# Performance work log

Measured on AMD Instinct MI355X. Metric: run time of the kernel, lower is better.

The kernel has to match this reference:

```python
import jax, jax.numpy as jnp
import numpy as np

B, S, D, H, L = 16, 1024, 512, 8, 3
NUM_Q, NUM_C, TOTAL_RES = 10000, 300, 2


def setup_inputs() -> dict:
    k = jax.random.split(jax.random.key(0), 20)
    n = lambda i, s, sc=0.02: jax.random.normal(k[i], s, jnp.float32) * sc
    z = lambda: jnp.zeros((D,), jnp.float32)
    o = lambda: jnp.ones((D,), jnp.float32)
    return {
        'in_ex': jax.random.randint(k[0], (B, S), 0, NUM_Q),
        'in_cat': jax.random.randint(k[1], (B, S), 0, NUM_C),
        'in_res': jax.random.randint(k[2], (B, S), 0, 2),
        'in_pos': n(3, (B, S, D)),
        'en_out': n(4, (B, S, D)),
        'E_res': n(5, (TOTAL_RES + 1, D)),
        'E_ex': n(6, (2 * NUM_Q + 1, D)),
        'E_cat': n(7, (2 * NUM_C + 1, D)),
        'g1': o(), 'be1': z(), 'g2': o(), 'be2': z(), 'g3': o(), 'be3': z(),
        'Wq1': n(8, (D, D)), 'bq1': z(), 'Wk1': n(9, (D, D)), 'bk1': z(),
        'Wv1': n(10, (D, D)), 'bv1': z(), 'Wo1': n(11, (D, D)), 'bo1': z(),
        'Wq2': n(12, (D, D)), 'bq2': z(), 'Wk2': n(13, (D, D)), 'bk2': z(),
        'Wv2': n(14, (D, D)), 'bv2': z(), 'Wo2': n(15, (D, D)), 'bo2': z(),
        'fW1': n(16, (D, D)), 'fb1': z(), 'fW2': n(17, (D, D)), 'fb2': z(),
    }


def layer_norm(x, g, b, eps=1e-5):
    m = x.mean(-1, keepdims=True)
    v = ((x - m) ** 2).mean(-1, keepdims=True)
    return (x - m) / jnp.sqrt(v + eps) * g + b


def pyr_attn(q_in, kv_in, Wq, bq, Wk, bk, Wv, bv, Wo, bo):
    # q_in, kv_in: (S, B, D) as in nn.MultiheadAttention convention
    Sq, Bq, Dm = q_in.shape
    dh = Dm // H
    heads = lambda x: x.reshape(x.shape[0], Bq, H, dh).transpose(1, 2, 0, 3)  # (B,H,S,dh)
    qh = heads(q_in @ Wq + bq)
    kh = heads(kv_in @ Wk + bk)
    vh = heads(kv_in @ Wv + bv)
    Skv = kv_in.shape[0]
    i = jnp.arange(Sq)[:, None]
    Ks, Vs, Ms = [], [], []
    for l in range(L):  # pyramid levels: keys/values avg-pooled by 2**l
        f = 2 ** l
        nb = Skv // f
        Ks.append(kh[:, :, :nb * f].reshape(Bq, H, nb, f, dh).mean(3))
        Vs.append(vh[:, :, :nb * f].reshape(Bq, H, nb, f, dh).mean(3))
        # causal: query i may attend pooled block j only if the block ends at or before i
        Ms.append(i >= (jnp.arange(nb)[None, :] + 1) * f - 1)
    K = jnp.concatenate(Ks, 2)
    V = jnp.concatenate(Vs, 2)
    M = jnp.concatenate(Ms, 1)  # (Sq, K_total) multi-level causal mask
    sc = jnp.einsum('bhqd,bhkd->bhqk', qh, K) / np.sqrt(dh).astype(np.float32)
    sc = jnp.where(M[None, None], sc, -1e9)
    a = jax.nn.softmax(sc, -1)
    out = jnp.einsum('bhqk,bhkd->bhqd', a, V)
    return out.transpose(2, 0, 1, 3).reshape(Sq, Bq, Dm) @ Wo + bo


def reference(in_ex, in_cat, in_res, in_pos, en_out, E_res, E_ex, E_cat,
              g1, be1, g2, be2, g3, be3,
              Wq1, bq1, Wk1, bk1, Wv1, bv1, Wo1, bo1,
              Wq2, bq2, Wk2, bk2, Wv2, bv2, Wo2, bo2,
              fW1, fb1, fW2, fb2):
    # embedding sum (first_block=True)
    out = E_res[in_res] + E_ex[in_ex + NUM_Q * in_res] + E_cat[in_cat + NUM_C * in_res] + in_pos
    out = out.transpose(1, 0, 2)  # (S, B, D)
    out = layer_norm(out, g1, be1)
    out = out + pyr_attn(out, out, Wq1, bq1, Wk1, bk1, Wv1, bv1, Wo1, bo1)
    en = layer_norm(en_out.transpose(1, 0, 2), g2, be2)
    out = out + pyr_attn(out, en, Wq2, bq2, Wk2, bk2, Wv2, bv2, Wo2, bo2)
    out = out.transpose(1, 0, 2)  # (B, S, D)
    out = layer_norm(out, g3, be3)
    out = out + (jax.nn.relu(out @ fW1 + fb1) @ fW2 + fb2)
    return out
```

## Files before the change

kernel.cpp:

```cpp
#include <hip/hip_runtime.h>


#define BB 16
#define SS 1024
#define DD 512
#define HH 8
#define DH 64
#define KTOT 1792
#define NROW (BB*SS)

typedef unsigned short u16;
typedef __attribute__((ext_vector_type(8))) u16 u16x8;
typedef __attribute__((ext_vector_type(4))) u16 u16x4;
typedef __attribute__((ext_vector_type(8))) short s16x8;
typedef __attribute__((ext_vector_type(4))) float f32x4;

__device__ __forceinline__ float b2f(u16 u) {
    return __uint_as_float(((unsigned int)u) << 16);
}
__device__ __forceinline__ u16 f2b(float f) {
    unsigned int u = __float_as_uint(f);
    return (u16)((u + 0x7FFF + ((u >> 16) & 1)) >> 16);
}
__device__ __forceinline__ s16x8 u2s8(u16x8 u) {
    union { u16x8 u; s16x8 s; } x; x.u = u; return x.s;
}
__device__ __forceinline__ f32x4 mfma16(s16x8 a, s16x8 b, f32x4 c) {
    return __builtin_amdgcn_mfma_f32_16x16x32_bf16(a, b, c, 0, 0, 0);
}
__device__ __forceinline__ float wave_sum(float v) {
    #pragma unroll
    for (int m = 1; m < 64; m <<= 1) v += __shfl_xor(v, m, 64);
    return v;
}

__global__ __launch_bounds__(256) void embed_ln_k(
    const int* __restrict__ in_ex, const int* __restrict__ in_cat,
    const int* __restrict__ in_res, const float* __restrict__ in_pos,
    const float* __restrict__ E_res, const float* __restrict__ E_ex,
    const float* __restrict__ E_cat, const float* __restrict__ g,
    const float* __restrict__ be, float* __restrict__ out)
{
    int wave = threadIdx.x >> 6, lane = threadIdx.x & 63;
    int row = blockIdx.x * 4 + wave;
    int res = in_res[row];
    int ex  = in_ex[row] + 10000 * res;
    int cat = in_cat[row] + 300 * res;
    int d0 = lane * 8;
    const float* pr = &E_res[(size_t)res * DD + d0];
    const float* pe = &E_ex[(size_t)ex * DD + d0];
    const float* pc = &E_cat[(size_t)cat * DD + d0];
    const float* pp = &in_pos[(size_t)row * DD + d0];
    float x[8]; float s = 0.f;
    #pragma unroll
    for (int j = 0; j < 8; j++) { x[j] = pr[j] + pe[j] + pc[j] + pp[j]; s += x[j]; }
    s = wave_sum(s);
    float mean = s * (1.0f / DD);
    float vs = 0.f;
    #pragma unroll
    for (int j = 0; j < 8; j++) { float d = x[j] - mean; vs += d * d; }
    vs = wave_sum(vs);
    float rstd = rsqrtf(vs * (1.0f / DD) + 1e-5f);
    #pragma unroll
    for (int j = 0; j < 8; j++)
        out[(size_t)row * DD + d0 + j] = (x[j] - mean) * rstd * g[d0 + j] + be[d0 + j];
}

template<bool OUTB>
__global__ __launch_bounds__(256) void ln_k(
    const float* __restrict__ x, const float* __restrict__ g,
    const float* __restrict__ be, void* __restrict__ outv)
{
    int wave = threadIdx.x >> 6, lane = threadIdx.x & 63;
    int row = blockIdx.x * 4 + wave;
    int d0 = lane * 8;
    const float* px = &x[(size_t)row * DD + d0];
    float xv[8]; float s = 0.f;
    #pragma unroll
    for (int j = 0; j < 8; j++) { xv[j] = px[j]; s += xv[j]; }
    s = wave_sum(s);
    float mean = s * (1.0f / DD);
    float vs = 0.f;
    #pragma unroll
    for (int j = 0; j < 8; j++) { float d = xv[j] - mean; vs += d * d; }
    vs = wave_sum(vs);
    float rstd = rsqrtf(vs * (1.0f / DD) + 1e-5f);
    #pragma unroll
    for (int j = 0; j < 8; j++) {
        float v = (xv[j] - mean) * rstd * g[d0 + j] + be[d0 + j];
        if (OUTB) ((u16*)outv)[(size_t)row * DD + d0 + j] = f2b(v);
        else      ((float*)outv)[(size_t)row * DD + d0 + j] = v;
    }
}

__global__ __launch_bounds__(256) void transpose_k(const float* __restrict__ src, u16* __restrict__ dst)
{
    int idx = blockIdx.x * 256 + threadIdx.x;
    int n = idx & 511, k = idx >> 9;
    dst[n * 512 + k] = f2b(src[k * 512 + n]);
}

__global__ __launch_bounds__(256) void pool_k12_k(u16* __restrict__ KP)
{
    int idx = blockIdx.x * 256 + threadIdx.x;
    int d = idx & 63;
    int t = idx >> 6;
    int k12 = t % 768;
    int bh = t / 768;
    int s0, f;
    if (k12 < 512) { s0 = 2 * k12; f = 2; } else { s0 = 4 * (k12 - 512); f = 4; }
    size_t base = (size_t)bh * KTOT * DH;
    float acc = 0.f;
    for (int i = 0; i < f; i++)
        acc += b2f(KP[base + (size_t)(s0 + i) * DH + d]);
    KP[base + (size_t)(1024 + k12) * DH + d] = f2b(acc * (1.0f / (float)f));
}

__global__ __launch_bounds__(256) void pool_vt_k(const u16* __restrict__ Vp, u16* __restrict__ VPt)
{
    __shared__ __align__(16) u16 T[64 * 72];
    int tid = threadIdx.x;
    int st = blockIdx.x;
    int h  = blockIdx.y;
    int b  = blockIdx.z;
    int s0 = st * 64;
    {
        const u16* src = &Vp[((size_t)(b * SS + s0)) * DD + h * DH];
        #pragma unroll
        for (int it = 0; it < 2; it++) {
            int idx = it * 256 + tid;
            int row = idx >> 3, unit = idx & 7;
            *(u16x8*)&T[row * 72 + unit * 8] =
                *(const u16x8*)&src[(size_t)row * DD + unit * 8];
        }
    }
    __syncthreads();
    int d = tid & 63, g = tid >> 6;
    size_t obase = ((size_t)(b * HH + h) * DH + d) * KTOT;
    #pragma unroll
    for (int gg = 0; gg < 2; gg++) {
        int grp = g * 2 + gg;
        u16x8 v;
        #pragma unroll
        for (int j = 0; j < 8; j++) v[j] = T[(grp * 8 + j) * 72 + d];
        *(u16x8*)&VPt[obase + s0 + grp * 8] = v;
    }
    {
        u16x8 v;
        #pragma unroll
        for (int j = 0; j < 8; j++) {
            int sl = g * 8 + j;
            float a = b2f(T[(2 * sl) * 72 + d]) + b2f(T[(2 * sl + 1) * 72 + d]);
            v[j] = f2b(a * 0.5f);
        }
        *(u16x8*)&VPt[obase + 1024 + st * 32 + g * 8] = v;
    }
    {
        u16x4 v;
        #pragma unroll
        for (int j = 0; j < 4; j++) {
            int s2 = g * 4 + j;
            float a = 0.f;
            #pragma unroll
            for (int i = 0; i < 4; i++) a += b2f(T[(4 * s2 + i) * 72 + d]);
            v[j] = f2b(a * 0.25f);
        }
        *(u16x4*)&VPt[obase + 1536 + st * 16 + g * 4] = v;
    }
}

template<bool AF32, bool RELU, bool RES, bool OUTB, bool KLAY>
__global__ __launch_bounds__(256) void gemm_k(
    const void* __restrict__ Av, const u16* __restrict__ Wt,
    const float* __restrict__ bias, const float* __restrict__ resid,
    void* __restrict__ Cv, int M, int K)
{
    const int N = 512;
    __shared__ __align__(16) u16 As[128 * 40];
    __shared__ __align__(16) u16 Bs[128 * 40];
    int tid = threadIdx.x;
    int wave = tid >> 6, lane = tid & 63;
    int quad = lane >> 4, l16 = lane & 15;
    int m0 = blockIdx.y * 128, n0 = blockIdx.x * 128;
    int wm = (wave >> 1) * 64, wn = (wave & 1) * 64;
    int r = tid >> 1, cg = (tid & 1) * 16;
    f32x4 acc[4][4];
    #pragma unroll
    for (int i = 0; i < 4; i++)
        #pragma unroll
        for (int j = 0; j < 4; j++)
            #pragma unroll
            for (int rr = 0; rr < 4; rr++) acc[i][j][rr] = 0.f;

    for (int k0 = 0; k0 < K; k0 += 32) {
        __syncthreads();
        if (AF32) {
            const float* src = &((const float*)Av)[(size_t)(m0 + r) * K + k0 + cg];
            u16x8 lo, hi;
            #pragma unroll
            for (int j = 0; j < 8; j++) { lo[j] = f2b(src[j]); hi[j] = f2b(src[j + 8]); }
            *(u16x8*)&As[r * 40 + cg] = lo;
            *(u16x8*)&As[r * 40 + cg + 8] = hi;
        } else {
            const u16* src = &((const u16*)Av)[(size_t)(m0 + r) * K + k0 + cg];
            *(u16x8*)&As[r * 40 + cg] = *(const u16x8*)&src[0];
            *(u16x8*)&As[r * 40 + cg + 8] = *(const u16x8*)&src[8];
        }
        {
            const u16* src = &Wt[(size_t)(n0 + r) * K + k0 + cg];
            *(u16x8*)&Bs[r * 40 + cg] = *(const u16x8*)&src[0];
            *(u16x8*)&Bs[r * 40 + cg + 8] = *(const u16x8*)&src[8];
        }
        __syncthreads();
        s16x8 af[4], bfr[4];
        #pragma unroll
        for (int i = 0; i < 4; i++)
            af[i] = u2s8(*(const u16x8*)&As[(wm + i * 16 + l16) * 40 + quad * 8]);
        #pragma unroll
        for (int j = 0; j < 4; j++)
            bfr[j] = u2s8(*(const u16x8*)&Bs[(wn + j * 16 + l16) * 40 + quad * 8]);
        #pragma unroll
        for (int i = 0; i < 4; i++)
            #pragma unroll
            for (int j = 0; j < 4; j++)
                acc[i][j] = mfma16(af[i], bfr[j], acc[i][j]);
    }

    #pragma unroll
    for (int j = 0; j < 4; j++) {
        int col = n0 + wn + j * 16 + l16;
        float bv = bias[col];
        #pragma unroll
        for (int i = 0; i < 4; i++) {
            int rowb = m0 + wm + i * 16 + quad * 4;
            #pragma unroll
            for (int rr = 0; rr < 4; rr++) {
                float v = acc[i][j][rr] + bv;
                if (RELU) v = fmaxf(v, 0.f);
                int row = rowb + rr;
                if (RES) v += resid[(size_t)row * N + col];
                if (KLAY) {
                    int b_ = row >> 10, s_ = row & 1023;
                    size_t dst = (((size_t)(b_ * HH + (col >> 6)) * KTOT) + s_) * DH + (col & 63);
                    ((u16*)Cv)[dst] = f2b(v);
                } else if (OUTB) {
                    ((u16*)Cv)[(size_t)row * N + col] = f2b(v);
                } else {
                    ((float*)Cv)[(size_t)row * N + col] = v;
                }
            }
        }
    }
}

__global__ __launch_bounds__(512) void attn_k(
    const u16* __restrict__ Qp, const u16* __restrict__ KP,
    const u16* __restrict__ VPt, u16* __restrict__ Hout)
{
    __shared__ __align__(16) u16 Ksh[64 * 72];
    __shared__ __align__(16) u16 Vsh[64 * 72];
    __shared__ float Sc[8][16 * 68];
    int tid = threadIdx.x;
    int wave = tid >> 6, lane = tid & 63;
    int quad = lane >> 4, l16 = lane & 15;
    int id = blockIdx.x;
    int h = id & 7;
    int inner = id >> 3;
    int x = inner & 3, b = inner >> 2;

    int t0 = x + 4 * wave;
    int tiles[2] = { t0, 63 - t0 };

    const u16* Kb = KP  + ((size_t)(b * HH + h)) * KTOT * DH;
    const u16* Vt = VPt + ((size_t)(b * HH + h)) * DH * KTOT;

    s16x8 qa[2][2];
    f32x4 o[2][4];
    float mrun[2] = {-INFINITY, -INFINITY}, lrun[2] = {0.f, 0.f};
    #pragma unroll
    for (int c = 0; c < 2; c++) {
        int q0 = tiles[c] * 16;
        const u16* qrow = Qp + ((size_t)(b * SS + q0 + l16)) * DD + h * DH;
        qa[c][0] = u2s8(*(const u16x8*)&qrow[quad * 8]);
        qa[c][1] = u2s8(*(const u16x8*)&qrow[32 + quad * 8]);
        #pragma unroll
        for (int j = 0; j < 4; j++)
            #pragma unroll
            for (int r = 0; r < 4; r++) o[c][j][r] = 0.f;
    }
    float* Sw = &Sc[wave][0];

    int srow = tid >> 3, sunit = tid & 7;
    u16x8 kreg = *(const u16x8*)&Kb[(size_t)tid * 8];
    u16x8 vreg = *(const u16x8*)&Vt[(size_t)srow * KTOT + sunit * 8];

    for (int ch = 0; ch < 28; ch++) {
        int kbase = ch * 64;
        int lv = (ch < 16) ? 0 : (ch < 24) ? 1 : 2;
        __syncthreads();
        *(u16x8*)&Ksh[srow * 72 + sunit * 8] = kreg;
        *(u16x8*)&Vsh[srow * 72 + sunit * 8] = vreg;
        __syncthreads();
        if (ch + 1 < 28) {
            int nb = (ch + 1) * 64;
            kreg = *(const u16x8*)&Kb[(size_t)nb * DH + tid * 8];
            vreg = *(const u16x8*)&Vt[(size_t)srow * KTOT + nb + sunit * 8];
        }

        #pragma unroll
        for (int c = 0; c < 2; c++) {
            int q0 = tiles[c] * 16;
            int qmax = q0 + 15;
            int efirst = (lv == 0) ? kbase
                       : (lv == 1) ? 2 * (kbase - 1024) + 1
                                   : 4 * (kbase - 1536) + 3;
            if (efirst > qmax) continue;

            #pragma unroll
            for (int t = 0; t < 4; t++) {
                const u16* kr = &Ksh[(t * 16 + l16) * 72];
                s16x8 kf0 = u2s8(*(const u16x8*)&kr[quad * 8]);
                s16x8 kf1 = u2s8(*(const u16x8*)&kr[32 + quad * 8]);
                f32x4 z;
                #pragma unroll
                for (int r = 0; r < 4; r++) z[r] = 0.f;
                z = mfma16(qa[c][0], kf0, z);
                z = mfma16(qa[c][1], kf1, z);
                int key = kbase + t * 16 + l16;
                int e = (lv == 0) ? key
                      : (lv == 1) ? 2 * (key - 1024) + 1
                                  : 4 * (key - 1536) + 3;
                #pragma unroll
                for (int r = 0; r < 4; r++) {
                    int q = q0 + quad * 4 + r;
                    Sw[(quad * 4 + r) * 68 + t * 16 + l16] =
                        (q >= e) ? z[r] * 0.125f : -1e30f;
                }
            }
            asm volatile("s_waitcnt lgkmcnt(0)" ::: "memory");

            float sv[16];
            {
                const float* base0 = &Sw[l16 * 68 + quad * 8];
                f32x4 a0 = *(const f32x4*)&base0[0];
                f32x4 a1 = *(const f32x4*)&base0[4];
                f32x4 a2 = *(const f32x4*)&base0[32];
                f32x4 a3 = *(const f32x4*)&base0[36];
                #pragma unroll
                for (int j = 0; j < 4; j++) {
                    sv[j] = a0[j]; sv[4 + j] = a1[j];
                    sv[8 + j] = a2[j]; sv[12 + j] = a3[j];
                }
            }

            float cmax = sv[0];
            #pragma unroll
            for (int j = 1; j < 16; j++) cmax = fmaxf(cmax, sv[j]);
            cmax = fmaxf(cmax, __shfl_xor(cmax, 16, 64));
            cmax = fmaxf(cmax, __shfl_xor(cmax, 32, 64));
            float newm = fmaxf(mrun[c], cmax);
            float al = __expf(mrun[c] - newm);
            float p[16]; float ps = 0.f;
            #pragma unroll
            for (int j = 0; j < 16; j++) { p[j] = __expf(sv[j] - newm); ps += p[j]; }
            ps += __shfl_xor(ps, 16, 64);
            ps += __shfl_xor(ps, 32, 64);
            lrun[c] = lrun[c] * al + ps;
            mrun[c] = newm;

            float alr[4];
            #pragma unroll
            for (int r = 0; r < 4; r++) alr[r] = __shfl(al, quad * 4 + r, 64);
            #pragma unroll
            for (int j = 0; j < 4; j++)
                #pragma unroll
                for (int r = 0; r < 4; r++) o[c][j][r] *= alr[r];

            u16x8 pk0, pk1;
            #pragma unroll
            for (int j = 0; j < 8; j++) { pk0[j] = f2b(p[j]); pk1[j] = f2b(p[8 + j]); }
            s16x8 pf0 = u2s8(pk0), pf1 = u2s8(pk1);

            #pragma unroll
            for (int j = 0; j < 4; j++) {
                const u16* vr = &Vsh[(j * 16 + l16) * 72];
                o[c][j] = mfma16(pf0, u2s8(*(const u16x8*)&vr[quad * 8]), o[c][j]);
                o[c][j] = mfma16(pf1, u2s8(*(const u16x8*)&vr[32 + quad * 8]), o[c][j]);
            }
        }
    }

    #pragma unroll
    for (int c = 0; c < 2; c++) {
        int q0 = tiles[c] * 16;
        float il = 1.0f / lrun[c];
        float ilr[4];
        #pragma unroll
        for (int r = 0; r < 4; r++) ilr[r] = __shfl(il, quad * 4 + r, 64);
        #pragma unroll
        for (int r = 0; r < 4; r++) {
            int q = q0 + quad * 4 + r;
            #pragma unroll
            for (int j = 0; j < 4; j++)
                Hout[((size_t)(b * SS + q)) * DD + h * DH + j * 16 + l16] = f2b(o[c][j][r] * ilr[r]);
        }
    }
}

extern "C" void kernel_launch(void* const* d_in, const int* in_sizes, int n_in,
                              void* d_out, int out_size, void* d_ws, size_t ws_size,
                              hipStream_t stream)
{
    (void)in_sizes; (void)n_in; (void)out_size; (void)ws_size;
    const int* in_ex  = (const int*)d_in[0];
    const int* in_cat = (const int*)d_in[1];
    const int* in_res = (const int*)d_in[2];
    const float* in_pos = (const float*)d_in[3];
    const float* en_out = (const float*)d_in[4];
    const float* E_res  = (const float*)d_in[5];
    const float* E_ex   = (const float*)d_in[6];
    const float* E_cat  = (const float*)d_in[7];
    const float* g1 = (const float*)d_in[8],  *be1 = (const float*)d_in[9];
    const float* g2 = (const float*)d_in[10], *be2 = (const float*)d_in[11];
    const float* g3 = (const float*)d_in[12], *be3 = (const float*)d_in[13];
    const float* Wq1 = (const float*)d_in[14], *bq1 = (const float*)d_in[15];
    const float* Wk1 = (const float*)d_in[16], *bk1 = (const float*)d_in[17];
    const float* Wv1 = (const float*)d_in[18], *bv1 = (const float*)d_in[19];
    const float* Wo1 = (const float*)d_in[20], *bo1 = (const float*)d_in[21];
    const float* Wq2 = (const float*)d_in[22], *bq2 = (const float*)d_in[23];
    const float* Wk2 = (const float*)d_in[24], *bk2 = (const float*)d_in[25];
    const float* Wv2 = (const float*)d_in[26], *bv2 = (const float*)d_in[27];
    const float* Wo2 = (const float*)d_in[28], *bo2 = (const float*)d_in[29];
    const float* fW1 = (const float*)d_in[30], *fb1 = (const float*)d_in[31];
    const float* fW2 = (const float*)d_in[32], *fb2 = (const float*)d_in[33];

    char* ws = (char*)d_ws;
    const size_t U = (size_t)NROW * DD * 2;
    float* x1 = (float*)(ws);
    u16* qb   = (u16*)(ws + 2 * U);
    u16* vb   = (u16*)(ws + 3 * U);
    u16* hb   = (u16*)(ws + 4 * U);
    u16* kp   = (u16*)(ws + 5 * U);
    u16* vpt  = (u16*)(ws + 5 * U + 7 * U / 4);
    u16* wt   = (u16*)(ws + 8 * U + U / 2);
    float* x2 = (float*)d_out;
    u16* en = (u16*)(ws);
    float* x3 = x1;
    float* x4 = (float*)(ws + 5 * U);
    u16* ff1 = hb;

    const float* wsrc[10] = {Wq1, Wk1, Wv1, Wo1, Wq2, Wk2, Wv2, Wo2, fW1, fW2};
    for (int i = 0; i < 10; i++)
        transpose_k<<<1024, 256, 0, stream>>>(wsrc[i], wt + (size_t)i * 262144);
    u16* tWq1 = wt,            *tWk1 = wt + 262144,   *tWv1 = wt + 2*262144, *tWo1 = wt + 3*262144;
    u16* tWq2 = wt + 4*262144, *tWk2 = wt + 5*262144, *tWv2 = wt + 6*262144, *tWo2 = wt + 7*262144;
    u16* tF1  = wt + 8*262144, *tF2  = wt + 9*262144;

    dim3 ggrid(4, 128);
    dim3 vtgrid(16, 8, 16);

    embed_ln_k<<<4096, 256, 0, stream>>>(in_ex, in_cat, in_res, in_pos,
                                         E_res, E_ex, E_cat, g1, be1, x1);

    gemm_k<true,false,false,true,false><<<ggrid, 256, 0, stream>>>(x1, tWq1, bq1, nullptr, qb, NROW, 512);
    gemm_k<true,false,false,true,true ><<<ggrid, 256, 0, stream>>>(x1, tWk1, bk1, nullptr, kp, NROW, 512);
    gemm_k<true,false,false,true,false><<<ggrid, 256, 0, stream>>>(x1, tWv1, bv1, nullptr, vb, NROW, 512);
    pool_k12_k<<<24576, 256, 0, stream>>>(kp);
    pool_vt_k<<<vtgrid, 256, 0, stream>>>(vb, vpt);
    attn_k<<<512, 512, 0, stream>>>(qb, kp, vpt, hb);
    gemm_k<false,false,true,false,false><<<ggrid, 256, 0, stream>>>(hb, tWo1, bo1, x1, x2, NROW, 512);

    ln_k<true><<<4096, 256, 0, stream>>>(en_out, g2, be2, en);
    gemm_k<true,false,false,true,false><<<ggrid, 256, 0, stream>>>(x2, tWq2, bq2, nullptr, qb, NROW, 512);
    gemm_k<false,false,false,true,true ><<<ggrid, 256, 0, stream>>>(en, tWk2, bk2, nullptr, kp, NROW, 512);
    gemm_k<false,false,false,true,false><<<ggrid, 256, 0, stream>>>(en, tWv2, bv2, nullptr, vb, NROW, 512);
    pool_k12_k<<<24576, 256, 0, stream>>>(kp);
    pool_vt_k<<<vtgrid, 256, 0, stream>>>(vb, vpt);
    attn_k<<<512, 512, 0, stream>>>(qb, kp, vpt, hb);
    gemm_k<false,false,true,false,false><<<ggrid, 256, 0, stream>>>(hb, tWo2, bo2, x2, x3, NROW, 512);

    ln_k<false><<<4096, 256, 0, stream>>>(x3, g3, be3, x4);
    gemm_k<true,true,false,true,false><<<ggrid, 256, 0, stream>>>(x4, tF1, fb1, nullptr, ff1, NROW, 512);
    gemm_k<false,false,true,false,false><<<ggrid, 256, 0, stream>>>(ff1, tF2, fb2, x4, (float*)d_out, NROW, 512);
}
```

Baseline: 737.9 us.

## Keep attention scores in registers via transposed MFMA and permuted key rows

The attention kernel no longer writes score tiles to shared memory and reads them back in a transposed layout. It computes K·Qᵀ with the MFMA operands swapped and a permuted key-row mapping, so each lane directly holds the scores it needs for the P·V MFMA, with the causal mask applied as a per-lane threshold. It also folds the 1/sqrt(dh) scale into a base-2 exponent via raw v_exp_f32, packs probabilities with v_cvt_pk_bf16_f32, and raises wave priority around MFMA sections. This removes LDS traffic and the wait that followed it, but the permutation must line the P fragments up with V rows, and the packing changes bf16 rounding behaviour.

Result: faster. 699.0 us (-5.3%).

```diff
diff --git a/kernel.cpp b/kernel.cpp
--- a/kernel.cpp
+++ b/kernel.cpp
@@ -32,6 +32,16 @@
     #pragma unroll
     for (int m = 1; m < 64; m <<= 1) v += __shfl_xor(v, m, 64);
     return v;
+}
+__device__ __forceinline__ float exp2a(float x) {
+    float r;
+    asm("v_exp_f32 %0, %1" : "=v"(r) : "v"(x));
+    return r;
+}
+__device__ __forceinline__ unsigned int cvtpk(float a, float b) {
+    unsigned int r;
+    asm("v_cvt_pk_bf16_f32 %0, %1, %2" : "=v"(r) : "v"(a), "v"(b));
+    return r;
 }
 
 __global__ __launch_bounds__(256) void embed_ln_k(
@@ -259,7 +269,6 @@
 {
     __shared__ __align__(16) u16 Ksh[64 * 72];
     __shared__ __align__(16) u16 Vsh[64 * 72];
-    __shared__ float Sc[8][16 * 68];
     int tid = threadIdx.x;
     int wave = tid >> 6, lane = tid & 63;
     int quad = lane >> 4, l16 = lane & 15;
@@ -288,7 +297,9 @@
             #pragma unroll
             for (int r = 0; r < 4; r++) o[c][j][r] = 0.f;
     }
-    float* Sw = &Sc[wave][0];
+
+    int row0 = 8 * (l16 >> 2) + (l16 & 3);
+    const float Cs = 0.18033688f;
 
     int srow = tid >> 3, sunit = tid & 7;
     u16x8 kreg = *(const u16x8*)&Kb[(size_t)tid * 8];
@@ -316,53 +327,51 @@
                                    : 4 * (kbase - 1536) + 3;
             if (efirst > qmax) continue;
 
+            int q = q0 + l16;
+            int kmax;
+            if (lv == 0)      kmax = q - kbase;
+            else if (lv == 1) kmax = ((q - 1) >> 1) - (kbase - 1024);
+            else              kmax = ((q - 3) >> 2) - (kbase - 1536);
+            int thrbase = kmax - 8 * quad;
+
+            float pz[4][4];
+            __builtin_amdgcn_s_setprio(1);
             #pragma unroll
             for (int t = 0; t < 4; t++) {
-                const u16* kr = &Ksh[(t * 16 + l16) * 72];
+                const int toff = (t & 1) * 4 + (t >> 1) * 32;
+                const u16* kr = &Ksh[(row0 + toff) * 72];
                 s16x8 kf0 = u2s8(*(const u16x8*)&kr[quad * 8]);
                 s16x8 kf1 = u2s8(*(const u16x8*)&kr[32 + quad * 8]);
                 f32x4 z;
                 #pragma unroll
                 for (int r = 0; r < 4; r++) z[r] = 0.f;
-                z = mfma16(qa[c][0], kf0, z);
-                z = mfma16(qa[c][1], kf1, z);
-                int key = kbase + t * 16 + l16;
-                int e = (lv == 0) ? key
-                      : (lv == 1) ? 2 * (key - 1024) + 1
-                                  : 4 * (key - 1536) + 3;
+                z = mfma16(kf0, qa[c][0], z);
+                z = mfma16(kf1, qa[c][1], z);
+                int thr = thrbase - toff;
                 #pragma unroll
-                for (int r = 0; r < 4; r++) {
-                    int q = q0 + quad * 4 + r;
-                    Sw[(quad * 4 + r) * 68 + t * 16 + l16] =
-                        (q >= e) ? z[r] * 0.125f : -1e30f;
-                }
+                for (int r = 0; r < 4; r++)
+                    pz[t][r] = (r <= thr) ? z[r] : -1e30f;
             }
-            asm volatile("s_waitcnt lgkmcnt(0)" ::: "memory");
-
-            float sv[16];
-            {
-                const float* base0 = &Sw[l16 * 68 + quad * 8];
-                f32x4 a0 = *(const f32x4*)&base0[0];
-                f32x4 a1 = *(const f32x4*)&base0[4];
-                f32x4 a2 = *(const f32x4*)&base0[32];
-                f32x4 a3 = *(const f32x4*)&base0[36];
-                #pragma unroll
-                for (int j = 0; j < 4; j++) {
-                    sv[j] = a0[j]; sv[4 + j] = a1[j];
-                    sv[8 + j] = a2[j]; sv[12 + j] = a3[j];
-                }
-            }
-
-            float cmax = sv[0];
-            #pragma unroll
-            for (int j = 1; j < 16; j++) cmax = fmaxf(cmax, sv[j]);
+            __builtin_amdgcn_s_setprio(0);
+
+            float a0 = fmaxf(fmaxf(pz[0][0], pz[0][1]), fmaxf(pz[0][2], pz[0][3]));
+            float a1 = fmaxf(fmaxf(pz[1][0], pz[1][1]), fmaxf(pz[1][2], pz[1][3]));
+            float a2 = fmaxf(fmaxf(pz[2][0], pz[2][1]), fmaxf(pz[2][2], pz[2][3]));
+            float a3 = fmaxf(fmaxf(pz[3][0], pz[3][1]), fmaxf(pz[3][2], pz[3][3]));
+            float cmax = fmaxf(fmaxf(a0, a1), fmaxf(a2, a3));
             cmax = fmaxf(cmax, __shfl_xor(cmax, 16, 64));
             cmax = fmaxf(cmax, __shfl_xor(cmax, 32, 64));
             float newm = fmaxf(mrun[c], cmax);
-            float al = __expf(mrun[c] - newm);
-            float p[16]; float ps = 0.f;
-            #pragma unroll
-            for (int j = 0; j < 16; j++) { p[j] = __expf(sv[j] - newm); ps += p[j]; }
+            float nmC = newm * Cs;
+            float al = exp2a((mrun[c] - newm) * Cs);
+            float p[4][4]; float ps = 0.f;
+            #pragma unroll
+            for (int t = 0; t < 4; t++)
+                #pragma unroll
+                for (int r = 0; r < 4; r++) {
+                    p[t][r] = exp2a(fmaf(pz[t][r], Cs, -nmC));
+                    ps += p[t][r];
+                }
             ps += __shfl_xor(ps, 16, 64);
             ps += __shfl_xor(ps, 32, 64);
             lrun[c] = lrun[c] * al + ps;
@@ -376,17 +385,21 @@
                 #pragma unroll
                 for (int r = 0; r < 4; r++) o[c][j][r] *= alr[r];
 
-            u16x8 pk0, pk1;
-            #pragma unroll
-            for (int j = 0; j < 8; j++) { pk0[j] = f2b(p[j]); pk1[j] = f2b(p[8 + j]); }
-            s16x8 pf0 = u2s8(pk0), pf1 = u2s8(pk1);
-
+            union { unsigned int w[4]; u16x8 v; } U0, U1;
+            U0.w[0] = cvtpk(p[0][0], p[0][1]); U0.w[1] = cvtpk(p[0][2], p[0][3]);
+            U0.w[2] = cvtpk(p[1][0], p[1][1]); U0.w[3] = cvtpk(p[1][2], p[1][3]);
+            U1.w[0] = cvtpk(p[2][0], p[2][1]); U1.w[1] = cvtpk(p[2][2], p[2][3]);
+            U1.w[2] = cvtpk(p[3][0], p[3][1]); U1.w[3] = cvtpk(p[3][2], p[3][3]);
+            s16x8 pf0 = u2s8(U0.v), pf1 = u2s8(U1.v);
+
+            __builtin_amdgcn_s_setprio(1);
             #pragma unroll
             for (int j = 0; j < 4; j++) {
                 const u16* vr = &Vsh[(j * 16 + l16) * 72];
                 o[c][j] = mfma16(pf0, u2s8(*(const u16x8*)&vr[quad * 8]), o[c][j]);
                 o[c][j] = mfma16(pf1, u2s8(*(const u16x8*)&vr[32 + quad * 8]), o[c][j]);
             }
+            __builtin_amdgcn_s_setprio(0);
         }
     }
 
```
